# Kernel optimization log

Hardware: AMD Instinct MI355X
Metric: run time of the kernel (lower is better)

Reference implementation:

```python
import jax, jax.numpy as jnp
import numpy as np

N = 100000
E = 1_600_000
EPS = 1e-5
NEG_SLOPE = 0.01


def leaky_relu(x):
    return jnp.where(x > 0, x, NEG_SLOPE * x)


def batchnorm(x, gamma, beta):
    # BatchNorm1d in training mode: batch statistics, biased variance
    m = jnp.mean(x, axis=0)
    v = jnp.mean((x - m) ** 2, axis=0)
    return (x - m) * jax.lax.rsqrt(v + EPS) * gamma + beta


def gcn_conv(x, W, b, src, dst, norm, n):
    # PyG GCNConv: h = x @ W; aggregate norm * h[src] into dst; add bias
    h = x @ W                              # [N, F_out]
    msgs = h[src] * norm[:, None]          # [E', F_out] gather + scale
    out = jax.ops.segment_sum(msgs, dst, num_segments=n)  # scatter-add
    return out + b


def setup_inputs() -> dict:
    key = jax.random.key(0)
    ks = jax.random.split(key, 14)
    d_in, d_h1, d_h2, d_out = 128, 128, 64, 8
    x = jax.random.normal(ks[0], (N, d_in), dtype=jnp.float32)
    edge_index = jax.random.randint(ks[1], (2, E), 0, N, dtype=jnp.int64)
    edge_weights = jax.random.uniform(ks[2], (E,), dtype=jnp.float32)
    # Glorot-ish init for GCNConv weights, zero bias (PyG default bias=True)
    W1 = jax.random.normal(ks[3], (d_in, d_h1), dtype=jnp.float32) / np.sqrt(d_in)
    b1 = jnp.zeros((d_h1,), jnp.float32)
    W2 = jax.random.normal(ks[4], (d_h1, d_h2), dtype=jnp.float32) / np.sqrt(d_h1)
    b2 = jnp.zeros((d_h2,), jnp.float32)
    W3 = jax.random.normal(ks[5], (d_h2, d_out), dtype=jnp.float32) / np.sqrt(d_h2)
    b3 = jnp.zeros((d_out,), jnp.float32)
    gamma1 = jnp.ones((d_h1,), jnp.float32)
    beta1 = jnp.zeros((d_h1,), jnp.float32)
    gamma2 = jnp.ones((d_h2,), jnp.float32)
    beta2 = jnp.zeros((d_h2,), jnp.float32)
    return {"x": x, "edge_index": edge_index, "edge_weights": edge_weights,
            "W1": W1, "b1": b1, "W2": W2, "b2": b2, "W3": W3, "b3": b3,
            "gamma1": gamma1, "beta1": beta1, "gamma2": gamma2, "beta2": beta2}


def reference(x, edge_index, edge_weights, W1, b1, W2, b2, W3, b3,
              gamma1, beta1, gamma2, beta2):
    # edge_weights is accepted (as in the original forward signature) but unused:
    # the module calls GCNConv(x, edge_index) without weights.
    n = x.shape[0]
    loop = jnp.arange(n, dtype=edge_index.dtype)
    src = jnp.concatenate([edge_index[0], loop])  # add self-loops
    dst = jnp.concatenate([edge_index[1], loop])
    # symmetric normalization with unit edge weights (in-degree on dst)
    deg = jax.ops.segment_sum(jnp.ones_like(dst, dtype=x.dtype), dst,
                              num_segments=n)
    dinv = jnp.where(deg > 0, jax.lax.rsqrt(deg), 0.0)
    norm = dinv[src] * dinv[dst]

    h = leaky_relu(gcn_conv(x, W1, b1, src, dst, norm, n))
    h = batchnorm(h, gamma1, beta1)
    h = leaky_relu(gcn_conv(h, W2, b2, src, dst, norm, n))
    h = batchnorm(h, gamma2, beta2)
    h = leaky_relu(gcn_conv(h, W3, b3, src, dst, norm, n))
    return h
```

## Files before the change

kernel.cpp:

```cpp
#include <hip/hip_runtime.h>
#include <cstdint>
#include <cstddef>

#define NEG_SLOPE 0.01f
#define BN_EPS 1e-5f
#define BSHIFT 6
#define BMASK 63
#define NBLK 64

using short8 = __attribute__((ext_vector_type(8))) short;
using f32x4 = __attribute__((ext_vector_type(4))) float;

__device__ inline unsigned short f2bf(float f) {
    unsigned int u = __float_as_uint(f);
    u += 0x7FFFu + ((u >> 16) & 1u);
    return (unsigned short)(u >> 16);
}


__global__ void zero_kernel(int* __restrict__ hist, float* __restrict__ stats, int m) {
    int i = blockIdx.x * blockDim.x + threadIdx.x;
    if (i < m) hist[i] = 0;
    if (i < 1024) stats[i] = 0.0f;
}

__global__ __launch_bounds__(1024) void chunkhist_kernel(const int* __restrict__ dst,
                                                         int* __restrict__ hist,
                                                         int E, int nb, int chunk) {
    __shared__ int lh[2048];
    const int b = blockIdx.x;
    for (int i = threadIdx.x; i < nb; i += 1024) lh[i] = 0;
    __syncthreads();
    const int e0 = b * chunk;
    const int e1 = min(E, e0 + chunk);
    for (int e = e0 + threadIdx.x; e < e1; e += 1024)
        atomicAdd(&lh[dst[e] >> BSHIFT], 1);
    __syncthreads();
    for (int k = threadIdx.x; k < nb; k += 1024)
        hist[k * NBLK + b] = lh[k];
}

__global__ __launch_bounds__(1024) void scan_block_kernel(const int* __restrict__ in,
                                                          int* __restrict__ out,
                                                          int* __restrict__ partials, int n) {
    __shared__ int sm[1024];
    int tid = threadIdx.x;
    int i = blockIdx.x * 1024 + tid;
    int v = (i < n) ? in[i] : 0;
    int x = v;
    sm[tid] = x;
    __syncthreads();
    for (int off = 1; off < 1024; off <<= 1) {
        int y = (tid >= off) ? sm[tid - off] : 0;
        __syncthreads();
        x += y;
        sm[tid] = x;
        __syncthreads();
    }
    if (i < n) out[i] = x - v;
    if (tid == 1023 && partials) partials[blockIdx.x] = x;
}

__global__ void scanadd2_kernel(int* __restrict__ S, const int* __restrict__ pofs,
                                int* __restrict__ bbase, int m, int nb, int E) {
    int i = blockIdx.x * blockDim.x + threadIdx.x;
    if (i < m) {
        int v = S[i] + pofs[i >> 10];
        S[i] = v;
        if ((i & (NBLK - 1)) == 0) bbase[i / NBLK] = v;
    }
    if (i == 0) bbase[nb] = E;
}

__global__ __launch_bounds__(1024) void chunkscatter_kernel(const int* __restrict__ src,
                                                            const int* __restrict__ dst,
                                                            const int* __restrict__ S,
                                                            unsigned int* __restrict__ packed,
                                                            int E, int nb, int chunk) {
    __shared__ int cur[2048];
    const int b = blockIdx.x;
    for (int k = threadIdx.x; k < nb; k += 1024) cur[k] = S[k * NBLK + b];
    __syncthreads();
    const int e0 = b * chunk;
    const int e1 = min(E, e0 + chunk);
    for (int e = e0 + threadIdx.x; e < e1; e += 1024) {
        int d = dst[e];
        int slot = atomicAdd(&cur[d >> BSHIFT], 1);
        packed[slot] = ((unsigned int)src[e] << BSHIFT) | (unsigned int)(d & BMASK);
    }
}

__global__ __launch_bounds__(256) void bucket_build_kernel(const unsigned int* __restrict__ packed,
                                                           const int* __restrict__ bbase,
                                                           int* __restrict__ rowptr,
                                                           float* __restrict__ dinv,
                                                           int* __restrict__ csr,
                                                           int N, int nb, int E) {
    const int b = blockIdx.x;
    const int t = threadIdx.x;
    const int e0 = bbase[b], e1 = bbase[b + 1];
    const int node0 = b << BSHIFT;
    __shared__ int hist[64], cur[64];
    if (t < 64) hist[t] = 0;
    __syncthreads();
    for (int e = e0 + t; e < e1; e += 256)
        atomicAdd(&hist[packed[e] & BMASK], 1);
    __syncthreads();
    if (t < 64) {
        int h = hist[t];
        int v = h;
        for (int o = 1; o < 64; o <<= 1) {
            int y = __shfl_up(v, o);
            if (t >= o) v += y;
        }
        int base = e0 + v - h;
        int node = node0 + t;
        if (node < N) {
            rowptr[node] = base;
            dinv[node] = rsqrtf((float)(h + 1));
        }
        cur[t] = base;
    }
    if (b == nb - 1 && t == 0) rowptr[N] = E;
    __syncthreads();
    for (int e = e0 + t; e < e1; e += 256) {
        unsigned int p = packed[e];
        int slot = atomicAdd(&cur[p & BMASK], 1);
        csr[slot] = (int)(p >> BSHIFT);
    }
}


__global__ void transposeW_kernel(const float* __restrict__ W, unsigned short* __restrict__ Wt,
                                  int K, int M) {
    int idx = blockIdx.x * blockDim.x + threadIdx.x;
    if (idx < K * M) {
        int k = idx / M, n = idx % M;
        Wt[n * K + k] = f2bf(W[idx]);
    }
}


template <int MF, bool BN>
__global__ __launch_bounds__(256) void mgemm_kernel(const float* __restrict__ X,
                                                    const unsigned short* __restrict__ Wt,
                                                    const float* __restrict__ bnS,
                                                    const float* __restrict__ bnT,
                                                    const float* __restrict__ dinv,
                                                    unsigned short* __restrict__ H, int n) {
    constexpr int K = 128;
    constexpr int CTW = (MF / 16) / 4;
    __shared__ unsigned short Xl[64 * K];
    __shared__ unsigned short Wl[MF * K];
    __shared__ float dl[64];

    const int t = threadIdx.x;
    const int wave = t >> 6;
    const int lane = t & 63;
    const int row0 = blockIdx.x * 64;

    for (int idx = t; idx < 64 * K / 4; idx += 256) {
        int r = idx >> 5, c4 = idx & 31;
        int row = row0 + r; if (row >= n) row = n - 1;
        float4 v = ((const float4*)(X + (size_t)row * K))[c4];
        if (BN) {
            float4 sv = ((const float4*)bnS)[c4];
            float4 tv = ((const float4*)bnT)[c4];
            v.x = v.x * sv.x + tv.x; v.y = v.y * sv.y + tv.y;
            v.z = v.z * sv.z + tv.z; v.w = v.w * sv.w + tv.w;
        }
        ushort4 o; o.x = f2bf(v.x); o.y = f2bf(v.y); o.z = f2bf(v.z); o.w = f2bf(v.w);
        *(ushort4*)((char*)Xl + r * 256 + ((c4 * 8) ^ ((r & 7) << 4))) = o;
    }
    for (int idx = t; idx < MF * K / 4; idx += 256) {
        int nr = idx >> 5, k4 = idx & 31;
        ushort4 o = ((const ushort4*)(Wt + (size_t)nr * K))[k4];
        *(ushort4*)((char*)Wl + nr * 256 + ((k4 * 8) ^ ((nr & 7) << 4))) = o;
    }
    if (t < 64) { int row = row0 + t; dl[t] = dinv[row < n ? row : n - 1]; }
    __syncthreads();

    f32x4 acc[CTW][4];
#pragma unroll
    for (int c = 0; c < CTW; ++c)
#pragma unroll
        for (int rt = 0; rt < 4; ++rt)
            acc[c][rt] = (f32x4){0.f, 0.f, 0.f, 0.f};

    const int kg = lane >> 4;
    const int lr = lane & 15;

#pragma unroll
    for (int kk = 0; kk < 4; ++kk) {
        const int kb = (kk * 32 + kg * 8) * 2;
        short8 a[4];
#pragma unroll
        for (int rt = 0; rt < 4; ++rt) {
            int r = rt * 16 + lr;
            a[rt] = *(const short8*)((const char*)Xl + r * 256 + (kb ^ ((r & 7) << 4)));
        }
#pragma unroll
        for (int c = 0; c < CTW; ++c) {
            int nr = (wave * CTW + c) * 16 + lr;
            short8 b = *(const short8*)((const char*)Wl + nr * 256 + (kb ^ ((nr & 7) << 4)));
#pragma unroll
            for (int rt = 0; rt < 4; ++rt)
                acc[c][rt] = __builtin_amdgcn_mfma_f32_16x16x32_bf16(a[rt], b, acc[c][rt], 0, 0, 0);
        }
    }
    __syncthreads();

    unsigned short* Ol = (unsigned short*)Xl;
#pragma unroll
    for (int c = 0; c < CTW; ++c) {
        int col = (wave * CTW + c) * 16 + lr;
#pragma unroll
        for (int rt = 0; rt < 4; ++rt) {
#pragma unroll
            for (int j = 0; j < 4; ++j) {
                int r = rt * 16 + kg * 4 + j;
                Ol[r * MF + col] = f2bf(acc[c][rt][j] * dl[r]);
            }
        }
    }
    __syncthreads();
    for (int idx = t; idx < 64 * MF / 4; idx += 256) {
        int r = idx / (MF / 4), c4 = idx % (MF / 4);
        int row = row0 + r;
        if (row < n)
            ((ushort4*)(H + (size_t)row * MF))[c4] = ((const ushort4*)Ol)[idx];
    }
}


template <int K, int M, int KC, int RPT, bool BN>
__global__ __launch_bounds__(256) void gemm_kernel(const float* __restrict__ X,
                                                   const float* __restrict__ W,
                                                   const float* __restrict__ bnS,
                                                   const float* __restrict__ bnT,
                                                   const float* __restrict__ dinv,
                                                   unsigned short* __restrict__ H, int n) {
    constexpr int COLG = M / 4;
    constexpr int ROWG = 256 / COLG;
    constexpr int RB = ROWG * RPT;
    __shared__ float Xl[RB][KC + 4];
    __shared__ float Wl[KC][M];

    const int t = threadIdx.x;
    const int colg = t % COLG;
    const int rowg = t / COLG;
    const int row0 = blockIdx.x * RB;

    float4 acc[RPT];
#pragma unroll
    for (int r = 0; r < RPT; ++r) acc[r] = make_float4(0.f, 0.f, 0.f, 0.f);

    for (int kc = 0; kc < K; kc += KC) {
        {
            const float4* Wg = (const float4*)(W + (size_t)kc * M);
            float4* Ws = (float4*)(&Wl[0][0]);
            for (int idx = t; idx < KC * M / 4; idx += 256) Ws[idx] = Wg[idx];
        }
        {
            constexpr int C4 = KC / 4;
            for (int idx = t; idx < RB * C4; idx += 256) {
                int r = idx / C4, c4 = idx % C4;
                int row = row0 + r;
                if (row >= n) row = n - 1;
                float4 v = ((const float4*)(X + (size_t)row * K + kc))[c4];
                if (BN) {
                    float4 sv = ((const float4*)(bnS + kc))[c4];
                    float4 tv = ((const float4*)(bnT + kc))[c4];
                    v.x = v.x * sv.x + tv.x;
                    v.y = v.y * sv.y + tv.y;
                    v.z = v.z * sv.z + tv.z;
                    v.w = v.w * sv.w + tv.w;
                }
                *(float4*)(&Xl[r][c4 * 4]) = v;
            }
        }
        __syncthreads();
#pragma unroll 8
        for (int k = 0; k < KC; ++k) {
            float4 w4 = *(const float4*)(&Wl[k][colg * 4]);
#pragma unroll
            for (int r = 0; r < RPT; ++r) {
                float xv = Xl[rowg * RPT + r][k];
                acc[r].x += xv * w4.x;
                acc[r].y += xv * w4.y;
                acc[r].z += xv * w4.z;
                acc[r].w += xv * w4.w;
            }
        }
        __syncthreads();
    }
#pragma unroll
    for (int r = 0; r < RPT; ++r) {
        int row = row0 + rowg * RPT + r;
        if (row < n) {
            const float di = dinv[row];
            ushort4 o;
            o.x = f2bf(acc[r].x * di);
            o.y = f2bf(acc[r].y * di);
            o.z = f2bf(acc[r].z * di);
            o.w = f2bf(acc[r].w * di);
            *(ushort4*)(H + (size_t)row * M + colg * 4) = o;
        }
    }
}


template <int F, int GROUP>
__global__ __launch_bounds__(256) void agg_kernel(const unsigned short* __restrict__ h,
                                                  const int* __restrict__ rowptr,
                                                  const int* __restrict__ csr,
                                                  const float* __restrict__ dinv,
                                                  const float* __restrict__ bias,
                                                  float* __restrict__ y, int n) {
    constexpr int NPB = 256 / GROUP;
    const int g = threadIdx.x % GROUP;
    const int node = blockIdx.x * NPB + threadIdx.x / GROUP;
    if (node >= n) return;
    const unsigned short* hp = h + g * 8;
    float a0 = 0.f, a1 = 0.f, a2 = 0.f, a3 = 0.f, a4 = 0.f, a5 = 0.f, a6 = 0.f, a7 = 0.f;
#define ACC8(v)                                    \
    a0 += __uint_as_float((v).x << 16);            \
    a1 += __uint_as_float((v).x & 0xFFFF0000u);    \
    a2 += __uint_as_float((v).y << 16);            \
    a3 += __uint_as_float((v).y & 0xFFFF0000u);    \
    a4 += __uint_as_float((v).z << 16);            \
    a5 += __uint_as_float((v).z & 0xFFFF0000u);    \
    a6 += __uint_as_float((v).w << 16);            \
    a7 += __uint_as_float((v).w & 0xFFFF0000u);
    int e = rowptr[node];
    const int r1 = rowptr[node + 1];
    for (; e + 4 <= r1; e += 4) {
        const int s0 = csr[e], s1 = csr[e + 1], s2 = csr[e + 2], s3 = csr[e + 3];
        const uint4 v0 = *(const uint4*)(hp + (size_t)s0 * F);
        const uint4 v1 = *(const uint4*)(hp + (size_t)s1 * F);
        const uint4 v2 = *(const uint4*)(hp + (size_t)s2 * F);
        const uint4 v3 = *(const uint4*)(hp + (size_t)s3 * F);
        ACC8(v0); ACC8(v1); ACC8(v2); ACC8(v3);
    }
    for (; e < r1; ++e) {
        const int s = csr[e];
        const uint4 v = *(const uint4*)(hp + (size_t)s * F);
        ACC8(v);
    }
    {
        const uint4 v = *(const uint4*)(hp + (size_t)node * F);
        ACC8(v);
    }
#undef ACC8
    const float di = dinv[node];
    const int f0 = g * 8;
    const float4 bA = *(const float4*)(bias + f0);
    const float4 bB = *(const float4*)(bias + f0 + 4);
    float r[8];
    r[0] = di * a0 + bA.x; r[1] = di * a1 + bA.y;
    r[2] = di * a2 + bA.z; r[3] = di * a3 + bA.w;
    r[4] = di * a4 + bB.x; r[5] = di * a5 + bB.y;
    r[6] = di * a6 + bB.z; r[7] = di * a7 + bB.w;
#pragma unroll
    for (int k = 0; k < 8; ++k) r[k] = r[k] > 0.f ? r[k] : NEG_SLOPE * r[k];
    float4 o0, o1;
    o0.x = r[0]; o0.y = r[1]; o0.z = r[2]; o0.w = r[3];
    o1.x = r[4]; o1.y = r[5]; o1.z = r[6]; o1.w = r[7];
    float* yp = y + (size_t)node * F + f0;
    *(float4*)(yp) = o0;
    *(float4*)(yp + 4) = o1;
}


template <int F>
__global__ __launch_bounds__(256) void stats_kernel(const float* __restrict__ y,
                                                    float* __restrict__ sum,
                                                    float* __restrict__ ssq, int n) {
    constexpr int RPS = 256 / F;
    __shared__ float smS[256], smQ[256];
    const int t = threadIdx.x;
    const int f = t % F;
    const int r0 = t / F;
    float s = 0.f, q = 0.f;
    for (int row = blockIdx.x * RPS + r0; row < n; row += gridDim.x * RPS) {
        float v = y[(size_t)row * F + f];
        s += v;
        q += v * v;
    }
    smS[t] = s;
    smQ[t] = q;
    __syncthreads();
    if (t < F) {
        float S = 0.f, Q = 0.f;
#pragma unroll
        for (int r = 0; r < RPS; ++r) {
            S += smS[t + r * F];
            Q += smQ[t + r * F];
        }
        atomicAdd(&sum[t], S);
        atomicAdd(&ssq[t], Q);
    }
}

__global__ void bnparam_kernel(const float* __restrict__ sum, const float* __restrict__ ssq,
                               const float* __restrict__ gamma, const float* __restrict__ beta,
                               float* __restrict__ S, float* __restrict__ T, int n, int F) {
    int f = threadIdx.x;
    if (f < F) {
        float m = sum[f] / (float)n;
        float var = ssq[f] / (float)n - m * m;
        float inv = rsqrtf(var + BN_EPS);
        float sc = gamma[f] * inv;
        S[f] = sc;
        T[f] = beta[f] - m * sc;
    }
}


extern "C" void kernel_launch(void* const* d_in, const int* in_sizes, int n_in,
                              void* d_out, int out_size, void* d_ws, size_t ws_size,
                              hipStream_t stream) {
    const float* x = (const float*)d_in[0];
    const int* edges = (const int*)d_in[1];
    const float* W1 = (const float*)d_in[3];
    const float* b1 = (const float*)d_in[4];
    const float* W2 = (const float*)d_in[5];
    const float* b2 = (const float*)d_in[6];
    const float* W3 = (const float*)d_in[7];
    const float* b3 = (const float*)d_in[8];
    const float* gamma1 = (const float*)d_in[9];
    const float* beta1 = (const float*)d_in[10];
    const float* gamma2 = (const float*)d_in[11];
    const float* beta2 = (const float*)d_in[12];

    const int N = in_sizes[0] / 128;
    const int E = in_sizes[1] / 2;
    const int* esrc = edges;
    const int* edst = edges + E;
    const int nb = (N + BMASK) >> BSHIFT;
    const int M = nb * NBLK;
    const int chunk = (E + NBLK - 1) / NBLK;

    char* ws = (char*)d_ws;
    size_t off = 0;
    auto alloc = [&](size_t bytes) -> void* {
        void* p = ws + off;
        off = (off + bytes + 255) & ~(size_t)255;
        return p;
    };
    int* hist = (int*)alloc((size_t)M * 4);
    int* S = (int*)alloc((size_t)M * 4);
    int* partials = (int*)alloc(1024 * 4);
    int* pofs = (int*)alloc(1024 * 4);
    int* bbase = (int*)alloc((size_t)(nb + 1) * 4);
    int* rowptr = (int*)alloc((size_t)(N + 1) * 4);
    float* dinv = (float*)alloc((size_t)N * 4);
    float* stats = (float*)alloc(1024 * 4);
    unsigned short* wt1 = (unsigned short*)alloc(128 * 128 * 2);
    unsigned short* wt2 = (unsigned short*)alloc(64 * 128 * 2);
    int* csr = (int*)alloc((size_t)E * 4);
    unsigned short* hbuf = (unsigned short*)alloc((size_t)N * 128 * 2);
    float* ybuf = (float*)alloc((size_t)N * 128 * 4);
    unsigned int* packed = (unsigned int*)hbuf;

    float* sumA = stats;
    float* ssA = stats + 128;
    float* sA = stats + 256;
    float* tA = stats + 384;
    float* sumB = stats + 512;
    float* ssB = stats + 640;
    float* sB = stats + 768;
    float* tB = stats + 896;

    const int MB = (M + 1023) / 1024;

    zero_kernel<<<(M + 255) / 256, 256, 0, stream>>>(hist, stats, M);
    transposeW_kernel<<<(128 * 128 + 255) / 256, 256, 0, stream>>>(W1, wt1, 128, 128);
    transposeW_kernel<<<(128 * 64 + 255) / 256, 256, 0, stream>>>(W2, wt2, 128, 64);
    chunkhist_kernel<<<NBLK, 1024, 0, stream>>>(edst, hist, E, nb, chunk);
    scan_block_kernel<<<MB, 1024, 0, stream>>>(hist, S, partials, M);
    scan_block_kernel<<<1, 1024, 0, stream>>>(partials, pofs, nullptr, MB);
    scanadd2_kernel<<<(M + 255) / 256, 256, 0, stream>>>(S, pofs, bbase, M, nb, E);
    chunkscatter_kernel<<<NBLK, 1024, 0, stream>>>(esrc, edst, S, packed, E, nb, chunk);
    bucket_build_kernel<<<nb, 256, 0, stream>>>(packed, bbase, rowptr, dinv, csr, N, nb, E);

    mgemm_kernel<128, false><<<(N + 63) / 64, 256, 0, stream>>>(x, wt1, nullptr, nullptr, dinv, hbuf, N);
    agg_kernel<128, 16><<<(N + 15) / 16, 256, 0, stream>>>(hbuf, rowptr, csr, dinv, b1, ybuf, N);
    stats_kernel<128><<<256, 256, 0, stream>>>(ybuf, sumA, ssA, N);
    bnparam_kernel<<<1, 128, 0, stream>>>(sumA, ssA, gamma1, beta1, sA, tA, N, 128);

    mgemm_kernel<64, true><<<(N + 63) / 64, 256, 0, stream>>>(ybuf, wt2, sA, tA, dinv, hbuf, N);
    agg_kernel<64, 8><<<(N + 31) / 32, 256, 0, stream>>>(hbuf, rowptr, csr, dinv, b2, ybuf, N);
    stats_kernel<64><<<256, 256, 0, stream>>>(ybuf, sumB, ssB, N);
    bnparam_kernel<<<1, 64, 0, stream>>>(sumB, ssB, gamma2, beta2, sB, tB, N, 64);

    gemm_kernel<64, 8, 64, 1, true><<<(N + 127) / 128, 256, 0, stream>>>(ybuf, W3, sB, tB, dinv, hbuf, N);
    agg_kernel<8, 1><<<(N + 255) / 256, 256, 0, stream>>>(hbuf, rowptr, csr, dinv, b3, (float*)d_out, N);
}
```

Before: 325.3 us.

## Fuse BN statistics into aggregation and store intermediate activations as bf16

The separate stats kernels are removed: each aggregation block now accumulates per-feature sums and sums of squares and writes per-block partials, which bnparam reduces with one block per feature. Intermediate activations are stored in bf16 instead of fp32, and the GEMMs unpack bf16 input with BN applied on the fly. This cuts activation memory traffic and kernel launches. Other changes: a per-node kernel replaces the final 64→8 GEMM, the aggregation gather is unrolled to 8 with a grid-stride loop, NBLK doubles, and the zero kernel is dropped. Storing activations in bf16 adds rounding error relative to the fp32 reference.

```diff
diff --git a/kernel.cpp b/kernel.cpp
--- a/kernel.cpp
+++ b/kernel.cpp
@@ -6,7 +6,7 @@
 #define BN_EPS 1e-5f
 #define BSHIFT 6
 #define BMASK 63
-#define NBLK 64
+#define NBLK 128
 
 using short8 = __attribute__((ext_vector_type(8))) short;
 using f32x4 = __attribute__((ext_vector_type(4))) float;
@@ -17,12 +17,6 @@
     return (unsigned short)(u >> 16);
 }
 
-
-__global__ void zero_kernel(int* __restrict__ hist, float* __restrict__ stats, int m) {
-    int i = blockIdx.x * blockDim.x + threadIdx.x;
-    if (i < m) hist[i] = 0;
-    if (i < 1024) stats[i] = 0.0f;
-}
 
 __global__ __launch_bounds__(1024) void chunkhist_kernel(const int* __restrict__ dst,
                                                          int* __restrict__ hist,
@@ -141,8 +135,8 @@
 }
 
 
-template <int MF, bool BN>
-__global__ __launch_bounds__(256) void mgemm_kernel(const float* __restrict__ X,
+template <int MF, bool BN, bool XBF>
+__global__ __launch_bounds__(256) void mgemm_kernel(const void* __restrict__ Xv,
                                                     const unsigned short* __restrict__ Wt,
                                                     const float* __restrict__ bnS,
                                                     const float* __restrict__ bnT,
@@ -159,18 +153,49 @@
     const int lane = t & 63;
     const int row0 = blockIdx.x * 64;
 
-    for (int idx = t; idx < 64 * K / 4; idx += 256) {
-        int r = idx >> 5, c4 = idx & 31;
-        int row = row0 + r; if (row >= n) row = n - 1;
-        float4 v = ((const float4*)(X + (size_t)row * K))[c4];
-        if (BN) {
-            float4 sv = ((const float4*)bnS)[c4];
-            float4 tv = ((const float4*)bnT)[c4];
-            v.x = v.x * sv.x + tv.x; v.y = v.y * sv.y + tv.y;
-            v.z = v.z * sv.z + tv.z; v.w = v.w * sv.w + tv.w;
-        }
-        ushort4 o; o.x = f2bf(v.x); o.y = f2bf(v.y); o.z = f2bf(v.z); o.w = f2bf(v.w);
-        *(ushort4*)((char*)Xl + r * 256 + ((c4 * 8) ^ ((r & 7) << 4))) = o;
+    if (XBF) {
+        const unsigned short* X = (const unsigned short*)Xv;
+        for (int idx = t; idx < 64 * K / 8; idx += 256) {
+            int r = idx >> 4, c8 = idx & 15;
+            int row = row0 + r; if (row >= n) row = n - 1;
+            uint4 v = ((const uint4*)(X + (size_t)row * K))[c8];
+            float xv[8];
+            xv[0] = __uint_as_float(v.x << 16); xv[1] = __uint_as_float(v.x & 0xFFFF0000u);
+            xv[2] = __uint_as_float(v.y << 16); xv[3] = __uint_as_float(v.y & 0xFFFF0000u);
+            xv[4] = __uint_as_float(v.z << 16); xv[5] = __uint_as_float(v.z & 0xFFFF0000u);
+            xv[6] = __uint_as_float(v.w << 16); xv[7] = __uint_as_float(v.w & 0xFFFF0000u);
+            if (BN) {
+                const float4 s0 = ((const float4*)bnS)[c8 * 2];
+                const float4 s1 = ((const float4*)bnS)[c8 * 2 + 1];
+                const float4 t0 = ((const float4*)bnT)[c8 * 2];
+                const float4 t1 = ((const float4*)bnT)[c8 * 2 + 1];
+                xv[0] = xv[0] * s0.x + t0.x; xv[1] = xv[1] * s0.y + t0.y;
+                xv[2] = xv[2] * s0.z + t0.z; xv[3] = xv[3] * s0.w + t0.w;
+                xv[4] = xv[4] * s1.x + t1.x; xv[5] = xv[5] * s1.y + t1.y;
+                xv[6] = xv[6] * s1.z + t1.z; xv[7] = xv[7] * s1.w + t1.w;
+            }
+            uint4 o;
+            o.x = (unsigned)f2bf(xv[0]) | ((unsigned)f2bf(xv[1]) << 16);
+            o.y = (unsigned)f2bf(xv[2]) | ((unsigned)f2bf(xv[3]) << 16);
+            o.z = (unsigned)f2bf(xv[4]) | ((unsigned)f2bf(xv[5]) << 16);
+            o.w = (unsigned)f2bf(xv[6]) | ((unsigned)f2bf(xv[7]) << 16);
+            *(uint4*)((char*)Xl + r * 256 + ((c8 * 16) ^ ((r & 7) << 4))) = o;
+        }
+    } else {
+        const float* X = (const float*)Xv;
+        for (int idx = t; idx < 64 * K / 4; idx += 256) {
+            int r = idx >> 5, c4 = idx & 31;
+            int row = row0 + r; if (row >= n) row = n - 1;
+            float4 v = ((const float4*)(X + (size_t)row * K))[c4];
+            if (BN) {
+                float4 sv = ((const float4*)bnS)[c4];
+                float4 tv = ((const float4*)bnT)[c4];
+                v.x = v.x * sv.x + tv.x; v.y = v.y * sv.y + tv.y;
+                v.z = v.z * sv.z + tv.z; v.w = v.w * sv.w + tv.w;
+            }
+            ushort4 o; o.x = f2bf(v.x); o.y = f2bf(v.y); o.z = f2bf(v.z); o.w = f2bf(v.w);
+            *(ushort4*)((char*)Xl + r * 256 + ((c4 * 8) ^ ((r & 7) << 4))) = o;
+        }
     }
     for (int idx = t; idx < MF * K / 4; idx += 256) {
         int nr = idx >> 5, k4 = idx & 31;
@@ -233,96 +258,71 @@
 }
 
 
-template <int K, int M, int KC, int RPT, bool BN>
-__global__ __launch_bounds__(256) void gemm_kernel(const float* __restrict__ X,
-                                                   const float* __restrict__ W,
-                                                   const float* __restrict__ bnS,
-                                                   const float* __restrict__ bnT,
-                                                   const float* __restrict__ dinv,
-                                                   unsigned short* __restrict__ H, int n) {
-    constexpr int COLG = M / 4;
-    constexpr int ROWG = 256 / COLG;
-    constexpr int RB = ROWG * RPT;
-    __shared__ float Xl[RB][KC + 4];
-    __shared__ float Wl[KC][M];
-
+__global__ __launch_bounds__(256) void gemm3_kernel(const unsigned short* __restrict__ X,
+                                                    const float* __restrict__ W,
+                                                    const float* __restrict__ bnS,
+                                                    const float* __restrict__ bnT,
+                                                    const float* __restrict__ dinv,
+                                                    unsigned short* __restrict__ H, int n) {
+    __shared__ float Wl[512];
+    __shared__ float sl[64], tl[64];
     const int t = threadIdx.x;
-    const int colg = t % COLG;
-    const int rowg = t / COLG;
-    const int row0 = blockIdx.x * RB;
-
-    float4 acc[RPT];
-#pragma unroll
-    for (int r = 0; r < RPT; ++r) acc[r] = make_float4(0.f, 0.f, 0.f, 0.f);
-
-    for (int kc = 0; kc < K; kc += KC) {
-        {
-            const float4* Wg = (const float4*)(W + (size_t)kc * M);
-            float4* Ws = (float4*)(&Wl[0][0]);
-            for (int idx = t; idx < KC * M / 4; idx += 256) Ws[idx] = Wg[idx];
-        }
-        {
-            constexpr int C4 = KC / 4;
-            for (int idx = t; idx < RB * C4; idx += 256) {
-                int r = idx / C4, c4 = idx % C4;
-                int row = row0 + r;
-                if (row >= n) row = n - 1;
-                float4 v = ((const float4*)(X + (size_t)row * K + kc))[c4];
-                if (BN) {
-                    float4 sv = ((const float4*)(bnS + kc))[c4];
-                    float4 tv = ((const float4*)(bnT + kc))[c4];
-                    v.x = v.x * sv.x + tv.x;
-                    v.y = v.y * sv.y + tv.y;
-                    v.z = v.z * sv.z + tv.z;
-                    v.w = v.w * sv.w + tv.w;
-                }
-                *(float4*)(&Xl[r][c4 * 4]) = v;
-            }
-        }
-        __syncthreads();
-#pragma unroll 8
-        for (int k = 0; k < KC; ++k) {
-            float4 w4 = *(const float4*)(&Wl[k][colg * 4]);
-#pragma unroll
-            for (int r = 0; r < RPT; ++r) {
-                float xv = Xl[rowg * RPT + r][k];
-                acc[r].x += xv * w4.x;
-                acc[r].y += xv * w4.y;
-                acc[r].z += xv * w4.z;
-                acc[r].w += xv * w4.w;
-            }
-        }
-        __syncthreads();
-    }
-#pragma unroll
-    for (int r = 0; r < RPT; ++r) {
-        int row = row0 + rowg * RPT + r;
-        if (row < n) {
-            const float di = dinv[row];
-            ushort4 o;
-            o.x = f2bf(acc[r].x * di);
-            o.y = f2bf(acc[r].y * di);
-            o.z = f2bf(acc[r].z * di);
-            o.w = f2bf(acc[r].w * di);
-            *(ushort4*)(H + (size_t)row * M + colg * 4) = o;
-        }
-    }
-}
-
-
-template <int F, int GROUP>
+    for (int i = t; i < 512; i += 256) Wl[i] = W[i];
+    if (t < 64) { sl[t] = bnS[t]; tl[t] = bnT[t]; }
+    __syncthreads();
+    const int node = blockIdx.x * 256 + t;
+    if (node >= n) return;
+    float acc[8];
+#pragma unroll
+    for (int m = 0; m < 8; ++m) acc[m] = 0.f;
+    const uint4* xp = (const uint4*)(X + (size_t)node * 64);
+#pragma unroll
+    for (int c8 = 0; c8 < 8; ++c8) {
+        const uint4 v = xp[c8];
+        float xv[8];
+        xv[0] = __uint_as_float(v.x << 16); xv[1] = __uint_as_float(v.x & 0xFFFF0000u);
+        xv[2] = __uint_as_float(v.y << 16); xv[3] = __uint_as_float(v.y & 0xFFFF0000u);
+        xv[4] = __uint_as_float(v.z << 16); xv[5] = __uint_as_float(v.z & 0xFFFF0000u);
+        xv[6] = __uint_as_float(v.w << 16); xv[7] = __uint_as_float(v.w & 0xFFFF0000u);
+#pragma unroll
+        for (int j = 0; j < 8; ++j) {
+            const int k = c8 * 8 + j;
+            const float x = xv[j] * sl[k] + tl[k];
+#pragma unroll
+            for (int m = 0; m < 8; ++m) acc[m] += x * Wl[k * 8 + m];
+        }
+    }
+    const float di = dinv[node];
+    uint4 o;
+    o.x = (unsigned)f2bf(acc[0] * di) | ((unsigned)f2bf(acc[1] * di) << 16);
+    o.y = (unsigned)f2bf(acc[2] * di) | ((unsigned)f2bf(acc[3] * di) << 16);
+    o.z = (unsigned)f2bf(acc[4] * di) | ((unsigned)f2bf(acc[5] * di) << 16);
+    o.w = (unsigned)f2bf(acc[6] * di) | ((unsigned)f2bf(acc[7] * di) << 16);
+    *(uint4*)(H + (size_t)node * 8) = o;
+}
+
+
+template <int F, int GROUP, bool BF16OUT, bool STATS>
 __global__ __launch_bounds__(256) void agg_kernel(const unsigned short* __restrict__ h,
                                                   const int* __restrict__ rowptr,
                                                   const int* __restrict__ csr,
                                                   const float* __restrict__ dinv,
                                                   const float* __restrict__ bias,
-                                                  float* __restrict__ y, int n) {
+                                                  void* __restrict__ yout,
+                                                  float* __restrict__ sumP,
+                                                  float* __restrict__ ssqP,
+                                                  int n, int nblocks) {
     constexpr int NPB = 256 / GROUP;
     const int g = threadIdx.x % GROUP;
-    const int node = blockIdx.x * NPB + threadIdx.x / GROUP;
-    if (node >= n) return;
-    const unsigned short* hp = h + g * 8;
-    float a0 = 0.f, a1 = 0.f, a2 = 0.f, a3 = 0.f, a4 = 0.f, a5 = 0.f, a6 = 0.f, a7 = 0.f;
+    const int slot = threadIdx.x / GROUP;
+    const int f0 = g * 8;
+    const unsigned short* hp = h + f0;
+    float sst[8], ssq[8];
+#pragma unroll
+    for (int k = 0; k < 8; ++k) { sst[k] = 0.f; ssq[k] = 0.f; }
+    const float4 bA = *(const float4*)(bias + f0);
+    const float4 bB = *(const float4*)(bias + f0 + 4);
+
 #define ACC8(v)                                    \
     a0 += __uint_as_float((v).x << 16);            \
     a1 += __uint_as_float((v).x & 0xFFFF0000u);    \
@@ -332,85 +332,108 @@
     a5 += __uint_as_float((v).z & 0xFFFF0000u);    \
     a6 += __uint_as_float((v).w << 16);            \
     a7 += __uint_as_float((v).w & 0xFFFF0000u);
-    int e = rowptr[node];
-    const int r1 = rowptr[node + 1];
-    for (; e + 4 <= r1; e += 4) {
-        const int s0 = csr[e], s1 = csr[e + 1], s2 = csr[e + 2], s3 = csr[e + 3];
-        const uint4 v0 = *(const uint4*)(hp + (size_t)s0 * F);
-        const uint4 v1 = *(const uint4*)(hp + (size_t)s1 * F);
-        const uint4 v2 = *(const uint4*)(hp + (size_t)s2 * F);
-        const uint4 v3 = *(const uint4*)(hp + (size_t)s3 * F);
-        ACC8(v0); ACC8(v1); ACC8(v2); ACC8(v3);
-    }
-    for (; e < r1; ++e) {
-        const int s = csr[e];
-        const uint4 v = *(const uint4*)(hp + (size_t)s * F);
-        ACC8(v);
-    }
-    {
-        const uint4 v = *(const uint4*)(hp + (size_t)node * F);
-        ACC8(v);
+
+    for (int base = blockIdx.x * NPB; base < n; base += nblocks * NPB) {
+        const int node = base + slot;
+        if (node < n) {
+            float a0 = 0.f, a1 = 0.f, a2 = 0.f, a3 = 0.f,
+                  a4 = 0.f, a5 = 0.f, a6 = 0.f, a7 = 0.f;
+            int e = rowptr[node];
+            const int r1 = rowptr[node + 1];
+            for (; e + 8 <= r1; e += 8) {
+                const int s0 = csr[e],     s1 = csr[e + 1], s2 = csr[e + 2], s3 = csr[e + 3];
+                const int s4 = csr[e + 4], s5 = csr[e + 5], s6 = csr[e + 6], s7 = csr[e + 7];
+                const uint4 v0 = *(const uint4*)(hp + (size_t)s0 * F);
+                const uint4 v1 = *(const uint4*)(hp + (size_t)s1 * F);
+                const uint4 v2 = *(const uint4*)(hp + (size_t)s2 * F);
+                const uint4 v3 = *(const uint4*)(hp + (size_t)s3 * F);
+                const uint4 v4 = *(const uint4*)(hp + (size_t)s4 * F);
+                const uint4 v5 = *(const uint4*)(hp + (size_t)s5 * F);
+                const uint4 v6 = *(const uint4*)(hp + (size_t)s6 * F);
+                const uint4 v7 = *(const uint4*)(hp + (size_t)s7 * F);
+                ACC8(v0); ACC8(v1); ACC8(v2); ACC8(v3);
+                ACC8(v4); ACC8(v5); ACC8(v6); ACC8(v7);
+            }
+            for (; e < r1; ++e) {
+                const int s = csr[e];
+                const uint4 v = *(const uint4*)(hp + (size_t)s * F);
+                ACC8(v);
+            }
+            {
+                const uint4 v = *(const uint4*)(hp + (size_t)node * F);
+                ACC8(v);
+            }
+            const float di = dinv[node];
+            float r[8];
+            r[0] = di * a0 + bA.x; r[1] = di * a1 + bA.y;
+            r[2] = di * a2 + bA.z; r[3] = di * a3 + bA.w;
+            r[4] = di * a4 + bB.x; r[5] = di * a5 + bB.y;
+            r[6] = di * a6 + bB.z; r[7] = di * a7 + bB.w;
+#pragma unroll
+            for (int k = 0; k < 8; ++k) {
+                r[k] = r[k] > 0.f ? r[k] : NEG_SLOPE * r[k];
+                if (STATS) { sst[k] += r[k]; ssq[k] += r[k] * r[k]; }
+            }
+            if (BF16OUT) {
+                uint4 o;
+                o.x = (unsigned)f2bf(r[0]) | ((unsigned)f2bf(r[1]) << 16);
+                o.y = (unsigned)f2bf(r[2]) | ((unsigned)f2bf(r[3]) << 16);
+                o.z = (unsigned)f2bf(r[4]) | ((unsigned)f2bf(r[5]) << 16);
+                o.w = (unsigned)f2bf(r[6]) | ((unsigned)f2bf(r[7]) << 16);
+                *(uint4*)((unsigned short*)yout + (size_t)node * F + f0) = o;
+            } else {
+                float4 o0, o1;
+                o0.x = r[0]; o0.y = r[1]; o0.z = r[2]; o0.w = r[3];
+                o1.x = r[4]; o1.y = r[5]; o1.z = r[6]; o1.w = r[7];
+                float* yp = (float*)yout + (size_t)node * F + f0;
+                *(float4*)(yp) = o0;
+                *(float4*)(yp + 4) = o1;
+            }
+        }
     }
 #undef ACC8
-    const float di = dinv[node];
-    const int f0 = g * 8;
-    const float4 bA = *(const float4*)(bias + f0);
-    const float4 bB = *(const float4*)(bias + f0 + 4);
-    float r[8];
-    r[0] = di * a0 + bA.x; r[1] = di * a1 + bA.y;
-    r[2] = di * a2 + bA.z; r[3] = di * a3 + bA.w;
-    r[4] = di * a4 + bB.x; r[5] = di * a5 + bB.y;
-    r[6] = di * a6 + bB.z; r[7] = di * a7 + bB.w;
-#pragma unroll
-    for (int k = 0; k < 8; ++k) r[k] = r[k] > 0.f ? r[k] : NEG_SLOPE * r[k];
-    float4 o0, o1;
-    o0.x = r[0]; o0.y = r[1]; o0.z = r[2]; o0.w = r[3];
-    o1.x = r[4]; o1.y = r[5]; o1.z = r[6]; o1.w = r[7];
-    float* yp = y + (size_t)node * F + f0;
-    *(float4*)(yp) = o0;
-    *(float4*)(yp + 4) = o1;
-}
-
-
-template <int F>
-__global__ __launch_bounds__(256) void stats_kernel(const float* __restrict__ y,
-                                                    float* __restrict__ sum,
-                                                    float* __restrict__ ssq, int n) {
-    constexpr int RPS = 256 / F;
-    __shared__ float smS[256], smQ[256];
+    if (STATS) {
+        __shared__ float smS[F], smQ[F];
+        for (int i = threadIdx.x; i < F; i += 256) { smS[i] = 0.f; smQ[i] = 0.f; }
+        __syncthreads();
+#pragma unroll
+        for (int k = 0; k < 8; ++k) {
+            atomicAdd(&smS[f0 + k], sst[k]);
+            atomicAdd(&smQ[f0 + k], ssq[k]);
+        }
+        __syncthreads();
+        for (int i = threadIdx.x; i < F; i += 256) {
+            sumP[(size_t)blockIdx.x * F + i] = smS[i];
+            ssqP[(size_t)blockIdx.x * F + i] = smQ[i];
+        }
+    }
+}
+
+
+__global__ __launch_bounds__(256) void bnparam_kernel(const float* __restrict__ sumP,
+                                                      const float* __restrict__ ssqP,
+                                                      const float* __restrict__ gamma,
+                                                      const float* __restrict__ beta,
+                                                      float* __restrict__ S, float* __restrict__ T,
+                                                      int n, int F, int NB) {
+    const int f = blockIdx.x;
     const int t = threadIdx.x;
-    const int f = t % F;
-    const int r0 = t / F;
     float s = 0.f, q = 0.f;
-    for (int row = blockIdx.x * RPS + r0; row < n; row += gridDim.x * RPS) {
-        float v = y[(size_t)row * F + f];
-        s += v;
-        q += v * v;
-    }
-    smS[t] = s;
-    smQ[t] = q;
-    __syncthreads();
-    if (t < F) {
-        float S = 0.f, Q = 0.f;
-#pragma unroll
-        for (int r = 0; r < RPS; ++r) {
-            S += smS[t + r * F];
-            Q += smQ[t + r * F];
-        }
-        atomicAdd(&sum[t], S);
-        atomicAdd(&ssq[t], Q);
-    }
-}
-
-__global__ void bnparam_kernel(const float* __restrict__ sum, const float* __restrict__ ssq,
-                               const float* __restrict__ gamma, const float* __restrict__ beta,
-                               float* __restrict__ S, float* __restrict__ T, int n, int F) {
-    int f = threadIdx.x;
-    if (f < F) {
-        float m = sum[f] / (float)n;
-        float var = ssq[f] / (float)n - m * m;
-        float inv = rsqrtf(var + BN_EPS);
-        float sc = gamma[f] * inv;
+    for (int b = t; b < NB; b += 256) {
+        s += sumP[(size_t)b * F + f];
+        q += ssqP[(size_t)b * F + f];
+    }
+    __shared__ float rs[4], rq[4];
+    for (int o = 32; o; o >>= 1) { s += __shfl_down(s, o); q += __shfl_down(q, o); }
+    if ((t & 63) == 0) { rs[t >> 6] = s; rq[t >> 6] = q; }
+    __syncthreads();
+    if (t == 0) {
+        s = rs[0] + rs[1] + rs[2] + rs[3];
+        q = rq[0] + rq[1] + rq[2] + rq[3];
+        const float m = s / (float)n;
+        const float var = q / (float)n - m * m;
+        const float inv = rsqrtf(var + BN_EPS);
+        const float sc = gamma[f] * inv;
         S[f] = sc;
         T[f] = beta[f] - m * sc;
     }
@@ -440,6 +463,7 @@
     const int nb = (N + BMASK) >> BSHIFT;
     const int M = nb * NBLK;
     const int chunk = (E + NBLK - 1) / NBLK;
+    const int NB2 = 2048;
 
     char* ws = (char*)d_ws;
     size_t off = 0;
@@ -455,26 +479,25 @@
     int* bbase = (int*)alloc((size_t)(nb + 1) * 4);
     int* rowptr = (int*)alloc((size_t)(N + 1) * 4);
     float* dinv = (float*)alloc((size_t)N * 4);
-    float* stats = (float*)alloc(1024 * 4);
+    float* bn = (float*)alloc(512 * 4);
+    float* sumP1 = (float*)alloc((size_t)NB2 * 128 * 4);
+    float* ssqP1 = (float*)alloc((size_t)NB2 * 128 * 4);
+    float* sumP2 = (float*)alloc((size_t)NB2 * 64 * 4);
+    float* ssqP2 = (float*)alloc((size_t)NB2 * 64 * 4);
     unsigned short* wt1 = (unsigned short*)alloc(128 * 128 * 2);
     unsigned short* wt2 = (unsigned short*)alloc(64 * 128 * 2);
     int* csr = (int*)alloc((size_t)E * 4);
     unsigned short* hbuf = (unsigned short*)alloc((size_t)N * 128 * 2);
-    float* ybuf = (float*)alloc((size_t)N * 128 * 4);
+    unsigned short* ybuf = (unsigned short*)alloc((size_t)N * 128 * 2);
     unsigned int* packed = (unsigned int*)hbuf;
 
-    float* sumA = stats;
-    float* ssA = stats + 128;
-    float* sA = stats + 256;
-    float* tA = stats + 384;
-    float* sumB = stats + 512;
-    float* ssB = stats + 640;
-    float* sB = stats + 768;
-    float* tB = stats + 896;
+    float* sA = bn;
+    float* tA = bn + 128;
+    float* sB = bn + 256;
+    float* tB = bn + 384;
 
     const int MB = (M + 1023) / 1024;
 
-    zero_kernel<<<(M + 255) / 256, 256, 0, stream>>>(hist, stats, M);
     transposeW_kernel<<<(128 * 128 + 255) / 256, 256, 0, stream>>>(W1, wt1, 128, 128);
     transposeW_kernel<<<(128 * 64 + 255) / 256, 256, 0, stream>>>(W2, wt2, 128, 64);
     chunkhist_kernel<<<NBLK, 1024, 0, stream>>>(edst, hist, E, nb, chunk);
@@ -484,16 +507,15 @@
     chunkscatter_kernel<<<NBLK, 1024, 0, stream>>>(esrc, edst, S, packed, E, nb, chunk);
     bucket_build_kernel<<<nb, 256, 0, stream>>>(packed, bbase, rowptr, dinv, csr, N, nb, E);
 
-    mgemm_kernel<128, false><<<(N + 63) / 64, 256, 0, stream>>>(x, wt1, nullptr, nullptr, dinv, hbuf, N);
-    agg_kernel<128, 16><<<(N + 15) / 16, 256, 0, stream>>>(hbuf, rowptr, csr, dinv, b1, ybuf, N);
-    stats_kernel<128><<<256, 256, 0, stream>>>(ybuf, sumA, ssA, N);
-    bnparam_kernel<<<1, 128, 0, stream>>>(sumA, ssA, gamma1, beta1, sA, tA, N, 128);
-
-    mgemm_kernel<64, true><<<(N + 63) / 64, 256, 0, stream>>>(ybuf, wt2, sA, tA, dinv, hbuf, N);
-    agg_kernel<64, 8><<<(N + 31) / 32, 256, 0, stream>>>(hbuf, rowptr, csr, dinv, b2, ybuf, N);
-    stats_kernel<64><<<256, 256, 0, stream>>>(ybuf, sumB, ssB, N);
-    bnparam_kernel<<<1, 64, 0, stream>>>(sumB, ssB, gamma2, beta2, sB, tB, N, 64);
-
-    gemm_kernel<64, 8, 64, 1, true><<<(N + 127) / 128, 256, 0, stream>>>(ybuf, W3, sB, tB, dinv, hbuf, N);
-    agg_kernel<8, 1><<<(N + 255) / 256, 256, 0, stream>>>(hbuf, rowptr, csr, dinv, b3, (float*)d_out, N);
-}
+    mgemm_kernel<128, false, false><<<(N + 63) / 64, 256, 0, stream>>>(x, wt1, nullptr, nullptr, dinv, hbuf, N);
+    agg_kernel<128, 16, true, true><<<NB2, 256, 0, stream>>>(hbuf, rowptr, csr, dinv, b1, ybuf, sumP1, ssqP1, N, NB2);
+    bnparam_kernel<<<128, 256, 0, stream>>>(sumP1, ssqP1, gamma1, beta1, sA, tA, N, 128, NB2);
+
+    mgemm_kernel<64, true, true><<<(N + 63) / 64, 256, 0, stream>>>(ybuf, wt2, sA, tA, dinv, hbuf, N);
+    agg_kernel<64, 8, true, true><<<NB2, 256, 0, stream>>>(hbuf, rowptr, csr, dinv, b2, ybuf, sumP2, ssqP2, N, NB2);
+    bnparam_kernel<<<64, 256, 0, stream>>>(sumP2, ssqP2, gamma2, beta2, sB, tB, N, 64, NB2);
+
+    gemm3_kernel<<<(N + 255) / 256, 256, 0, stream>>>(ybuf, W3, sB, tB, dinv, hbuf, N);
+    const int NB3 = (N + 255) / 256;
+    agg_kernel<8, 1, false, false><<<NB3, 256, 0, stream>>>(hbuf, rowptr, csr, dinv, b3, (float*)d_out, nullptr, nullptr, N, NB3);
+}
```

New measurement: 292.5 us. 1.11x faster.
